# Kernel optimization log

Hardware: AMD Instinct MI355X
Metric: run time of the kernel (lower is better)

## Reference

```python
import jax, jax.numpy as jnp
import numpy as np

B, L, D1, D2 = 4, 2048, 1024, 1024

def setup_inputs() -> dict:
    key = jax.random.key(0)
    k1, k2, k3, k4, k5, k6 = jax.random.split(key, 6)
    s1 = 1.0 / np.sqrt(D1)
    s2 = 1.0 / np.sqrt(D2)
    return {
        "features_1": jax.random.normal(k1, (B, L, D1), dtype=jnp.float32),
        "features_2": jax.random.normal(k2, (B, L, D2), dtype=jnp.float32),
        # nn.Linear(d1, d2): W1 [d2, d1], b1 [d2]
        "W1": jax.random.uniform(k3, (D2, D1), jnp.float32, -s1, s1),
        "b1": jax.random.uniform(k4, (D2,), jnp.float32, -s1, s1),
        # nn.Linear(d2, d1): W2 [d1, d2], b2 [d1]
        "W2": jax.random.uniform(k5, (D1, D2), jnp.float32, -s2, s2),
        "b2": jax.random.uniform(k6, (D1,), jnp.float32, -s2, s2),
    }

def reference(features_1, features_2, W1, b1, W2, b2):
    # transformed_features_1: [B, L, D2]
    t1 = jnp.einsum('bld,ed->ble', features_1, W1) + b1
    # unscaled similarity: [B, L, L]
    sim = jnp.einsum('ble,bme->blm', t1, features_2)
    attn = jax.nn.softmax(sim, axis=-1)  # both softmaxes are identical
    attended_1 = jnp.einsum('blm,bme->ble', attn, features_2)  # [B, L, D2]
    attended_2 = jnp.einsum('blm,bme->ble', attn, t1)          # [B, L, D2]
    attended_2 = jnp.einsum('ble,de->bld', attended_2, W2) + b2  # [B, L, D1]
    return attended_1, attended_2
```

## Files before the change

kernel.cpp:

```cpp
#include <hip/hip_runtime.h>
#include <stdint.h>

#define BB 4
#define LL 2048
#define DD 1024

typedef __attribute__((ext_vector_type(4))) float f32x4;
typedef __attribute__((ext_vector_type(8))) _Float16 f16x8;
typedef __attribute__((ext_vector_type(4))) unsigned short u16x4;
typedef __attribute__((ext_vector_type(8))) unsigned short u16x8;
typedef unsigned short u16;

__device__ __forceinline__ u16 f2h(float x){
  return __builtin_bit_cast(u16, (_Float16)x);
}
__device__ __forceinline__ float h2f(u16 h){
  return (float)__builtin_bit_cast(_Float16, h);
}

__device__ __forceinline__ void gload16(const u16* g, u16* l){
  __builtin_amdgcn_global_load_lds((const __attribute__((address_space(1))) unsigned*)g,
                                   (__attribute__((address_space(3))) unsigned*)l,
                                   16, 0, 0);
}

__device__ __forceinline__ int xcd_swz(int bx, int nwg){
  return (bx & 7) * (nwg >> 3) + (bx >> 3);
}

__device__ __forceinline__ void stage_tile8(u16* lds, const u16* src, int ld, int wave, int lane){
  const int r0 = lane >> 3;
  const int cs = (((lane & 7) ^ r0) << 3);
  #pragma unroll
  for (int j = 0; j < 2; ++j){
    const int rb = wave*16 + j*8;
    gload16(src + (size_t)(rb + r0)*ld + cs, lds + rb*64);
  }
}

__device__ __forceinline__ void stage_fatA(u16* lds, const u16* src, int ld, int wave, int lane){
  const int r0 = lane >> 3;
  const int cs = (((lane & 7) ^ r0) << 3);
  #pragma unroll
  for (int j = 0; j < 8; ++j){
    const int rb = wave*64 + j*8;
    gload16(src + (size_t)(rb + r0)*ld + cs, lds + rb*64);
  }
}
__device__ __forceinline__ void stage_fatB(u16* lds, const u16* src, int ld, int wave, int lane){
  const int r0 = lane >> 3;
  const int cs = (((lane & 7) ^ r0) << 3);
  #pragma unroll
  for (int j = 0; j < 4; ++j){
    const int rb = wave*32 + j*8;
    gload16(src + (size_t)(rb + r0)*ld + cs, lds + rb*64);
  }
}

__device__ __forceinline__ f16x8 frag_ld(const u16* t, int row, int ko){
  return __builtin_bit_cast(f16x8,
    *reinterpret_cast<const f32x4*>(t + row*64 + (ko ^ ((row & 7) << 3))));
}

__global__ void cast_all_k(const float* __restrict__ f2, u16* __restrict__ f2f,
                           u16* __restrict__ f2T,
                           const float* __restrict__ f1, u16* __restrict__ f1f,
                           const float* __restrict__ W1, u16* __restrict__ w1f,
                           const float* __restrict__ W2, u16* __restrict__ w2f){
  __shared__ u16 t[32][33];
  const int z = blockIdx.z;
  if (z < 4){
    const int d0 = blockIdx.x*32, l0 = blockIdx.y*32;
    const float* src = f2 + (size_t)z*LL*DD;
    u16* d1 = f2f + (size_t)z*LL*DD;
    u16* d2 = f2T + (size_t)z*DD*LL;
    const int x = threadIdx.x;
    for (int j = threadIdx.y; j < 32; j += 8){
      u16 h = f2h(src[(size_t)(l0+j)*DD + d0 + x]);
      d1[(size_t)(l0+j)*DD + d0 + x] = h;
      t[j][x] = h;
    }
    __syncthreads();
    for (int j = threadIdx.y; j < 32; j += 8)
      d2[(size_t)(d0+j)*LL + l0 + x] = t[x][j];
  } else {
    const int n1 = (BB*LL*DD)/4, nw = (DD*DD)/4;
    const int ntot = n1 + 2*nw;
    const int base = (blockIdx.y*32 + blockIdx.x)*256 + threadIdx.y*32 + threadIdx.x;
    const int stride = 2048*256;
    for (int i = base; i < ntot; i += stride){
      const float* s; u16* d; int k;
      if (i < n1){ s = f1; d = f1f; k = i; }
      else if (i < n1 + nw){ s = W1; d = w1f; k = i - n1; }
      else { s = W2; d = w2f; k = i - n1 - nw; }
      f32x4 v = reinterpret_cast<const f32x4*>(s)[k];
      u16x4 h;
      #pragma unroll
      for (int j = 0; j < 4; ++j) h[j] = f2h(v[j]);
      reinterpret_cast<u16x4*>(d)[k] = h;
    }
  }
}

__global__ __launch_bounds__(512,4) void gemm_t1_k(
    const u16* __restrict__ A_g, const u16* __restrict__ B_g,
    const float* __restrict__ bias, u16* __restrict__ Oh){
  __shared__ __align__(16) u16 As[128*64];
  __shared__ __align__(16) u16 Bs[128*64];
  const int bx = xcd_swz(blockIdx.x, gridDim.x);
  const int bm = bx >> 3, bn = bx & 7;
  const int tid = threadIdx.x, wave = tid>>6, lane = tid&63;
  const int wr = wave>>2, wc = wave&3;
  const u16* Ab = A_g + (size_t)(bm*128)*DD;
  const u16* Bb = B_g + (size_t)(bn*128)*DD;
  f32x4 acc[4][2];
  #pragma unroll
  for (int i=0;i<4;i++)
    #pragma unroll
    for (int j=0;j<2;j++) acc[i][j] = (f32x4){0.f,0.f,0.f,0.f};

  for (int k0 = 0; k0 < DD; k0 += 64){
    __syncthreads();
    stage_tile8(As, Ab + k0, DD, wave, lane);
    stage_tile8(Bs, Bb + k0, DD, wave, lane);
    __syncthreads();
    #pragma unroll
    for (int kk=0;kk<2;kk++){
      const int ko = kk*32 + ((lane>>4)<<3);
      f16x8 a[4], bb[2];
      #pragma unroll
      for (int mi=0;mi<4;mi++) a[mi]  = frag_ld(As, wr*64 + mi*16 + (lane&15), ko);
      #pragma unroll
      for (int ni=0;ni<2;ni++) bb[ni] = frag_ld(Bs, wc*32 + ni*16 + (lane&15), ko);
      #pragma unroll
      for (int mi=0;mi<4;mi++)
        #pragma unroll
        for (int ni=0;ni<2;ni++)
          acc[mi][ni] = __builtin_amdgcn_mfma_f32_16x16x32_f16(a[mi], bb[ni], acc[mi][ni], 0,0,0);
    }
  }
  #pragma unroll
  for (int mi=0;mi<4;mi++)
    #pragma unroll
    for (int ni=0;ni<2;ni++){
      const int r = bm*128 + wr*64 + mi*16 + ((lane>>4)<<2);
      const int c = bn*128 + wc*32 + ni*16 + (lane&15);
      const float bv = bias[c];
      #pragma unroll
      for (int j=0;j<4;j++)
        Oh[(size_t)(r+j)*DD + c] = f2h(acc[mi][ni][j] + bv);
    }
}

__global__ __launch_bounds__(512,4) void gemm_zt_k(const u16* __restrict__ t1f,
                                                   const u16* __restrict__ w2f,
                                                   u16* __restrict__ ZT){
  __shared__ __align__(16) u16 As[128*64];
  __shared__ __align__(16) u16 Bs[128*64];
  __shared__ u16 T[128*132];
  const int bx = xcd_swz(blockIdx.x, gridDim.x);
  const int bm = bx >> 3, bn = bx & 7;
  const int tid = threadIdx.x, wave = tid>>6, lane = tid&63;
  const int wr = wave>>2, wc = wave&3;
  const u16* Ab = t1f + (size_t)(bm*128)*DD;
  const u16* Bb = w2f + (size_t)(bn*128)*DD;
  f32x4 acc[4][2];
  #pragma unroll
  for (int i=0;i<4;i++)
    #pragma unroll
    for (int j=0;j<2;j++) acc[i][j] = (f32x4){0.f,0.f,0.f,0.f};

  for (int k0 = 0; k0 < DD; k0 += 64){
    __syncthreads();
    stage_tile8(As, Ab + k0, DD, wave, lane);
    stage_tile8(Bs, Bb + k0, DD, wave, lane);
    __syncthreads();
    #pragma unroll
    for (int kk=0;kk<2;kk++){
      const int ko = kk*32 + ((lane>>4)<<3);
      f16x8 a[4], bb[2];
      #pragma unroll
      for (int mi=0;mi<4;mi++) a[mi]  = frag_ld(As, wr*64 + mi*16 + (lane&15), ko);
      #pragma unroll
      for (int ni=0;ni<2;ni++) bb[ni] = frag_ld(Bs, wc*32 + ni*16 + (lane&15), ko);
      #pragma unroll
      for (int mi=0;mi<4;mi++)
        #pragma unroll
        for (int ni=0;ni<2;ni++)
          acc[mi][ni] = __builtin_amdgcn_mfma_f32_16x16x32_f16(a[mi], bb[ni], acc[mi][ni], 0,0,0);
    }
  }
  #pragma unroll
  for (int mi=0;mi<4;mi++)
    #pragma unroll
    for (int ni=0;ni<2;ni++){
      const int r = wr*64 + mi*16 + ((lane>>4)<<2);
      const int c = wc*32 + ni*16 + (lane&15);
      #pragma unroll
      for (int j=0;j<4;j++)
        T[(r+j)*132 + c] = f2h(acc[mi][ni][j]);
    }
  __syncthreads();
  const int b2i = bm >> 4;
  const int mb  = (bm*128) & 2047;
  const int d   = tid >> 2, m0 = (tid & 3) << 5;
  u16* dst = ZT + ((size_t)b2i*DD + bn*128 + d)*LL + mb + m0;
  #pragma unroll
  for (int g = 0; g < 4; ++g){
    u16x8 v;
    #pragma unroll
    for (int e = 0; e < 8; ++e) v[e] = T[(m0 + g*8 + e)*132 + d];
    *reinterpret_cast<u16x8*>(dst + g*8) = v;
  }
}

__global__ __launch_bounds__(256) void softmax_k(u16* __restrict__ sim){
  const int row = blockIdx.x;
  u16* p = sim + (size_t)row * LL;
  const int tid = threadIdx.x, wave = tid>>6, lane = tid&63;
  u16x8 v = reinterpret_cast<const u16x8*>(p)[tid];
  float x[8];
  #pragma unroll
  for (int j=0;j<8;j++) x[j] = h2f(v[j]);
  float mx = fmaxf(fmaxf(fmaxf(x[0],x[1]), fmaxf(x[2],x[3])),
                   fmaxf(fmaxf(x[4],x[5]), fmaxf(x[6],x[7])));
  #pragma unroll
  for (int o = 32; o; o >>= 1) mx = fmaxf(mx, __shfl_xor(mx, o, 64));
  __shared__ float red[8];
  if (lane == 0) red[wave] = mx;
  __syncthreads();
  mx = fmaxf(fmaxf(red[0], red[1]), fmaxf(red[2], red[3]));
  float e[8], s = 0.f;
  #pragma unroll
  for (int j=0;j<8;j++){ e[j] = __expf(x[j]-mx); s += e[j]; }
  #pragma unroll
  for (int o = 32; o; o >>= 1) s += __shfl_xor(s, o, 64);
  if (lane == 0) red[4+wave] = s;
  __syncthreads();
  s = (red[4]+red[5]) + (red[6]+red[7]);
  const float inv = 1.0f / s;
  u16x8 w;
  #pragma unroll
  for (int j=0;j<8;j++) w[j] = f2h(e[j]*inv);
  reinterpret_cast<u16x8*>(p)[tid] = w;
}

template<int EPI>
__global__ __launch_bounds__(256,2) void gemmf_k(
    const u16* __restrict__ A_g, long long sAb, int lda,
    const u16* __restrict__ B0_g, const u16* __restrict__ B1_g, long long sBb, int ldb,
    float* __restrict__ C0, float* __restrict__ C1, long long sCb, int ldc,
    const float* __restrict__ bias, int K, int tn_sh){
  __shared__ __align__(16) u16 As[256*64];
  __shared__ __align__(16) u16 Bs[128*64];
  const int b = blockIdx.y;
  const int bx = xcd_swz(blockIdx.x, gridDim.x);
  const int bm = bx >> tn_sh, bn = bx & ((1 << tn_sh) - 1);
  const int tid = threadIdx.x, wave = tid>>6, lane = tid&63;
  const int wm = wave >> 1, wn = wave & 1;
  const u16* Ab = A_g + (size_t)b*sAb + (size_t)(bm*256)*lda;
  const u16* Bb;
  if (EPI == 1){
    Bb = ((bn < 8) ? B0_g : B1_g) + (size_t)b*sBb + (size_t)((bn&7)*128)*ldb;
  } else {
    Bb = B0_g + (size_t)b*sBb + (size_t)(bn*128)*ldb;
  }
  f32x4 acc[8][4];
  #pragma unroll
  for (int i=0;i<8;i++)
    #pragma unroll
    for (int j=0;j<4;j++) acc[i][j] = (f32x4){0.f,0.f,0.f,0.f};

  for (int k0 = 0; k0 < K; k0 += 64){
    __syncthreads();
    stage_fatA(As, Ab + k0, lda, wave, lane);
    stage_fatB(Bs, Bb + k0, ldb, wave, lane);
    __syncthreads();
    #pragma unroll
    for (int kk=0;kk<2;kk++){
      const int ko = kk*32 + ((lane>>4)<<3);
      f16x8 af[8], bf[4];
      #pragma unroll
      for (int mi=0;mi<8;mi++) af[mi] = frag_ld(As, wm*128 + mi*16 + (lane&15), ko);
      #pragma unroll
      for (int ni=0;ni<4;ni++) bf[ni] = frag_ld(Bs, wn*64 + ni*16 + (lane&15), ko);
      #pragma unroll
      for (int mi=0;mi<8;mi++)
        #pragma unroll
        for (int ni=0;ni<4;ni++)
          acc[mi][ni] = __builtin_amdgcn_mfma_f32_16x16x32_f16(af[mi], bf[ni], acc[mi][ni], 0,0,0);
    }
  }

  if (EPI == 2){
    u16* Oh = reinterpret_cast<u16*>(C0) + (size_t)b*sCb;
    #pragma unroll
    for (int mi=0;mi<8;mi++)
      #pragma unroll
      for (int ni=0;ni<4;ni++){
        const int r = bm*256 + wm*128 + mi*16 + ((lane>>4)<<2);
        const int c = bn*128 + wn*64 + ni*16 + (lane&15);
        #pragma unroll
        for (int j=0;j<4;j++)
          Oh[(size_t)(r+j)*ldc + c] = f2h(acc[mi][ni][j]);
      }
  } else {
    float* O = ((bn < 8) ? C0 : C1) + (size_t)b*sCb;
    const bool has_bias = (bn >= 8);
    #pragma unroll
    for (int mi=0;mi<8;mi++)
      #pragma unroll
      for (int ni=0;ni<4;ni++){
        const int r = bm*256 + wm*128 + mi*16 + ((lane>>4)<<2);
        const int c = (bn&7)*128 + wn*64 + ni*16 + (lane&15);
        const float bv = has_bias ? bias[c] : 0.f;
        #pragma unroll
        for (int j=0;j<4;j++)
          __builtin_nontemporal_store(acc[mi][ni][j] + bv, &O[(size_t)(r+j)*ldc + c]);
      }
  }
}

extern "C" void kernel_launch(void* const* d_in, const int* in_sizes, int n_in,
                              void* d_out, int out_size, void* d_ws, size_t ws_size,
                              hipStream_t stream) {
  const float* f1 = (const float*)d_in[0];
  const float* f2 = (const float*)d_in[1];
  const float* W1 = (const float*)d_in[2];
  const float* b1 = (const float*)d_in[3];
  const float* W2 = (const float*)d_in[4];
  const float* b2 = (const float*)d_in[5];
  float* out1 = (float*)d_out;
  float* out2 = out1 + (size_t)BB*LL*DD;

  char* ws = (char*)d_ws;
  u16* t1f = (u16*)(ws + 0);
  u16* ZT  = (u16*)(ws + 16777216);
  u16* f2f = (u16*)(ws + 33554432);
  u16* f2T = (u16*)(ws + 50331648);
  u16* w1f = (u16*)(ws + 67108864);
  u16* w2f = (u16*)(ws + 69206016);
  u16* sim = (u16*)(ws + 71303168);
  u16* f1f = (u16*)(ws + 71303168);

  cast_all_k<<<dim3(32, 64, 5), dim3(32, 8), 0, stream>>>(f2, f2f, f2T,
                                                          f1, f1f, W1, w1f, W2, w2f);
  gemm_t1_k<<<dim3(512, 1), 512, 0, stream>>>(f1f, w1f, b1, t1f);
  gemmf_k<2><<<dim3(128, BB), 256, 0, stream>>>(t1f, (long long)LL*DD, DD,
                                                f2f, nullptr, (long long)LL*DD, DD,
                                                (float*)sim, nullptr, (long long)LL*LL, LL,
                                                nullptr, DD, 4);
  softmax_k<<<BB*LL, 256, 0, stream>>>(sim);
  gemm_zt_k<<<dim3(512, 1), 512, 0, stream>>>(t1f, w2f, ZT);
  gemmf_k<1><<<dim3(128, BB), 256, 0, stream>>>(sim, (long long)LL*LL, LL,
                                                f2T, ZT, (long long)DD*LL, LL,
                                                out1, out2, (long long)LL*DD, DD,
                                                b2, LL, 4);
}
```

Baseline: 188.5 us.

## Precompute W2·W1 to fuse t1 and Z GEMMs into one pass over f1

Computes W12 = W2·W1 and a folded bias b2 + W2·b1 in small kernels, then a single GEMM kernel reads f1 once and produces both t1 (with W1) and Z^T (with W12). This drops the separate gemm_zt pass that re-read t1 and lets the final attention GEMM use the folded bias. It also adds a transposed cast of W1 and switches the output stores from nontemporal to regular stores. Z is now built from f1 rather than from the fp16-rounded t1, which changes rounding, and the fused kernel uses more LDS and registers per block.

```diff
diff --git a/kernel.cpp b/kernel.cpp
--- a/kernel.cpp
+++ b/kernel.cpp
@@ -64,16 +64,19 @@
 
 __global__ void cast_all_k(const float* __restrict__ f2, u16* __restrict__ f2f,
                            u16* __restrict__ f2T,
+                           const float* __restrict__ W1, u16* __restrict__ w1f,
+                           u16* __restrict__ w1T,
                            const float* __restrict__ f1, u16* __restrict__ f1f,
-                           const float* __restrict__ W1, u16* __restrict__ w1f,
                            const float* __restrict__ W2, u16* __restrict__ w2f){
   __shared__ u16 t[32][33];
   const int z = blockIdx.z;
-  if (z < 4){
+  if (z < 4 || z == 4){
+    const float* src; u16* d1; u16* d2; int nrow, ldT;
+    if (z < 4){ src = f2 + (size_t)z*LL*DD; d1 = f2f + (size_t)z*LL*DD;
+                d2 = f2T + (size_t)z*DD*LL; nrow = LL; ldT = LL; }
+    else      { src = W1; d1 = w1f; d2 = w1T; nrow = DD; ldT = DD; }
     const int d0 = blockIdx.x*32, l0 = blockIdx.y*32;
-    const float* src = f2 + (size_t)z*LL*DD;
-    u16* d1 = f2f + (size_t)z*LL*DD;
-    u16* d2 = f2T + (size_t)z*DD*LL;
+    if (l0 >= nrow) return;
     const int x = threadIdx.x;
     for (int j = threadIdx.y; j < 32; j += 8){
       u16 h = f2h(src[(size_t)(l0+j)*DD + d0 + x]);
@@ -82,17 +85,16 @@
     }
     __syncthreads();
     for (int j = threadIdx.y; j < 32; j += 8)
-      d2[(size_t)(d0+j)*LL + l0 + x] = t[x][j];
+      d2[(size_t)(d0+j)*ldT + l0 + x] = t[x][j];
   } else {
     const int n1 = (BB*LL*DD)/4, nw = (DD*DD)/4;
-    const int ntot = n1 + 2*nw;
+    const int ntot = n1 + nw;
     const int base = (blockIdx.y*32 + blockIdx.x)*256 + threadIdx.y*32 + threadIdx.x;
     const int stride = 2048*256;
     for (int i = base; i < ntot; i += stride){
       const float* s; u16* d; int k;
       if (i < n1){ s = f1; d = f1f; k = i; }
-      else if (i < n1 + nw){ s = W1; d = w1f; k = i - n1; }
-      else { s = W2; d = w2f; k = i - n1 - nw; }
+      else { s = W2; d = w2f; k = i - n1; }
       f32x4 v = reinterpret_cast<const f32x4*>(s)[k];
       u16x4 h;
       #pragma unroll
@@ -102,9 +104,26 @@
   }
 }
 
-__global__ __launch_bounds__(512,4) void gemm_t1_k(
-    const u16* __restrict__ A_g, const u16* __restrict__ B_g,
-    const float* __restrict__ bias, u16* __restrict__ Oh){
+__global__ __launch_bounds__(512) void bz2_k(const float* __restrict__ W2,
+                                             const float* __restrict__ b1,
+                                             const float* __restrict__ b2,
+                                             float* __restrict__ bz2){
+  const int wave = threadIdx.x >> 6, lane = threadIdx.x & 63;
+  const int d = blockIdx.x*8 + wave;
+  float s = 0.f;
+  #pragma unroll
+  for (int k = 0; k < 16; ++k){
+    const int e = lane + (k << 6);
+    s += W2[(size_t)d*DD + e] * b1[e];
+  }
+  #pragma unroll
+  for (int o = 32; o; o >>= 1) s += __shfl_xor(s, o, 64);
+  if (lane == 0) bz2[d] = b2[d] + s;
+}
+
+__global__ __launch_bounds__(512,4) void w12_k(const u16* __restrict__ A_g,
+                                               const u16* __restrict__ B_g,
+                                               u16* __restrict__ Oh){
   __shared__ __align__(16) u16 As[128*64];
   __shared__ __align__(16) u16 Bs[128*64];
   const int bx = xcd_swz(blockIdx.x, gridDim.x);
@@ -118,7 +137,6 @@
   for (int i=0;i<4;i++)
     #pragma unroll
     for (int j=0;j<2;j++) acc[i][j] = (f32x4){0.f,0.f,0.f,0.f};
-
   for (int k0 = 0; k0 < DD; k0 += 64){
     __syncthreads();
     stage_tile8(As, Ab + k0, DD, wave, lane);
@@ -145,51 +163,74 @@
     for (int ni=0;ni<2;ni++){
       const int r = bm*128 + wr*64 + mi*16 + ((lane>>4)<<2);
       const int c = bn*128 + wc*32 + ni*16 + (lane&15);
-      const float bv = bias[c];
       #pragma unroll
       for (int j=0;j<4;j++)
-        Oh[(size_t)(r+j)*DD + c] = f2h(acc[mi][ni][j] + bv);
-    }
-}
-
-__global__ __launch_bounds__(512,4) void gemm_zt_k(const u16* __restrict__ t1f,
-                                                   const u16* __restrict__ w2f,
-                                                   u16* __restrict__ ZT){
-  __shared__ __align__(16) u16 As[128*64];
-  __shared__ __align__(16) u16 Bs[128*64];
-  __shared__ u16 T[128*132];
+        Oh[(size_t)(r+j)*DD + c] = f2h(acc[mi][ni][j]);
+    }
+}
+
+__global__ __launch_bounds__(512,4) void t1z_k(const u16* __restrict__ f1f,
+                                               const u16* __restrict__ w1f,
+                                               const u16* __restrict__ w12f,
+                                               const float* __restrict__ b1,
+                                               u16* __restrict__ t1f,
+                                               u16* __restrict__ ZT){
+  __shared__ __align__(16) u16 SH[3*128*64];
+  u16* As  = SH;
+  u16* B1s = SH + 8192;
+  u16* B2s = SH + 16384;
   const int bx = xcd_swz(blockIdx.x, gridDim.x);
   const int bm = bx >> 3, bn = bx & 7;
   const int tid = threadIdx.x, wave = tid>>6, lane = tid&63;
   const int wr = wave>>2, wc = wave&3;
-  const u16* Ab = t1f + (size_t)(bm*128)*DD;
-  const u16* Bb = w2f + (size_t)(bn*128)*DD;
-  f32x4 acc[4][2];
+  const u16* Ab  = f1f  + (size_t)(bm*128)*DD;
+  const u16* B1b = w1f  + (size_t)(bn*128)*DD;
+  const u16* B2b = w12f + (size_t)(bn*128)*DD;
+  f32x4 acc1[4][2], acc2[4][2];
   #pragma unroll
   for (int i=0;i<4;i++)
     #pragma unroll
-    for (int j=0;j<2;j++) acc[i][j] = (f32x4){0.f,0.f,0.f,0.f};
+    for (int j=0;j<2;j++){ acc1[i][j] = (f32x4){0.f,0.f,0.f,0.f}; acc2[i][j] = acc1[i][j]; }
 
   for (int k0 = 0; k0 < DD; k0 += 64){
     __syncthreads();
-    stage_tile8(As, Ab + k0, DD, wave, lane);
-    stage_tile8(Bs, Bb + k0, DD, wave, lane);
+    stage_tile8(As,  Ab  + k0, DD, wave, lane);
+    stage_tile8(B1s, B1b + k0, DD, wave, lane);
+    stage_tile8(B2s, B2b + k0, DD, wave, lane);
     __syncthreads();
     #pragma unroll
     for (int kk=0;kk<2;kk++){
       const int ko = kk*32 + ((lane>>4)<<3);
-      f16x8 a[4], bb[2];
+      f16x8 a[4], b1v[2], b2v[2];
       #pragma unroll
       for (int mi=0;mi<4;mi++) a[mi]  = frag_ld(As, wr*64 + mi*16 + (lane&15), ko);
       #pragma unroll
-      for (int ni=0;ni<2;ni++) bb[ni] = frag_ld(Bs, wc*32 + ni*16 + (lane&15), ko);
+      for (int ni=0;ni<2;ni++){
+        b1v[ni] = frag_ld(B1s, wc*32 + ni*16 + (lane&15), ko);
+        b2v[ni] = frag_ld(B2s, wc*32 + ni*16 + (lane&15), ko);
+      }
       #pragma unroll
       for (int mi=0;mi<4;mi++)
         #pragma unroll
-        for (int ni=0;ni<2;ni++)
-          acc[mi][ni] = __builtin_amdgcn_mfma_f32_16x16x32_f16(a[mi], bb[ni], acc[mi][ni], 0,0,0);
-    }
-  }
+        for (int ni=0;ni<2;ni++){
+          acc1[mi][ni] = __builtin_amdgcn_mfma_f32_16x16x32_f16(a[mi], b1v[ni], acc1[mi][ni], 0,0,0);
+          acc2[mi][ni] = __builtin_amdgcn_mfma_f32_16x16x32_f16(a[mi], b2v[ni], acc2[mi][ni], 0,0,0);
+        }
+    }
+  }
+  #pragma unroll
+  for (int mi=0;mi<4;mi++)
+    #pragma unroll
+    for (int ni=0;ni<2;ni++){
+      const int r = bm*128 + wr*64 + mi*16 + ((lane>>4)<<2);
+      const int c = bn*128 + wc*32 + ni*16 + (lane&15);
+      const float bv = b1[c];
+      #pragma unroll
+      for (int j=0;j<4;j++)
+        t1f[(size_t)(r+j)*DD + c] = f2h(acc1[mi][ni][j] + bv);
+    }
+  __syncthreads();
+  u16* T = SH;
   #pragma unroll
   for (int mi=0;mi<4;mi++)
     #pragma unroll
@@ -198,7 +239,7 @@
       const int c = wc*32 + ni*16 + (lane&15);
       #pragma unroll
       for (int j=0;j<4;j++)
-        T[(r+j)*132 + c] = f2h(acc[mi][ni][j]);
+        T[(r+j)*132 + c] = f2h(acc2[mi][ni][j]);
     }
   __syncthreads();
   const int b2i = bm >> 4;
@@ -316,7 +357,7 @@
         const float bv = has_bias ? bias[c] : 0.f;
         #pragma unroll
         for (int j=0;j<4;j++)
-          __builtin_nontemporal_store(acc[mi][ni][j] + bv, &O[(size_t)(r+j)*ldc + c]);
+          O[(size_t)(r+j)*ldc + c] = acc[mi][ni][j] + bv;
       }
   }
 }
@@ -341,19 +382,24 @@
   u16* w1f = (u16*)(ws + 67108864);
   u16* w2f = (u16*)(ws + 69206016);
   u16* sim = (u16*)(ws + 71303168);
-  u16* f1f = (u16*)(ws + 71303168);
-
-  cast_all_k<<<dim3(32, 64, 5), dim3(32, 8), 0, stream>>>(f2, f2f, f2T,
-                                                          f1, f1f, W1, w1f, W2, w2f);
-  gemm_t1_k<<<dim3(512, 1), 512, 0, stream>>>(f1f, w1f, b1, t1f);
+  u16* f1f  = (u16*)(ws + 71303168);
+  u16* w1T  = (u16*)(ws + 71303168 + 16777216);
+  u16* w12f = (u16*)(ws + 71303168 + 18874368);
+  float* bz2 = (float*)(ws + 104857600);
+
+  cast_all_k<<<dim3(32, 64, 6), dim3(32, 8), 0, stream>>>(f2, f2f, f2T,
+                                                          W1, w1f, w1T,
+                                                          f1, f1f, W2, w2f);
+  bz2_k<<<128, 512, 0, stream>>>(W2, b1, b2, bz2);
+  w12_k<<<64, 512, 0, stream>>>(w2f, w1T, w12f);
+  t1z_k<<<512, 512, 0, stream>>>(f1f, w1f, w12f, b1, t1f, ZT);
   gemmf_k<2><<<dim3(128, BB), 256, 0, stream>>>(t1f, (long long)LL*DD, DD,
                                                 f2f, nullptr, (long long)LL*DD, DD,
                                                 (float*)sim, nullptr, (long long)LL*LL, LL,
                                                 nullptr, DD, 4);
   softmax_k<<<BB*LL, 256, 0, stream>>>(sim);
-  gemm_zt_k<<<dim3(512, 1), 512, 0, stream>>>(t1f, w2f, ZT);
   gemmf_k<1><<<dim3(128, BB), 256, 0, stream>>>(sim, (long long)LL*LL, LL,
                                                 f2T, ZT, (long long)DD*LL, LL,
                                                 out1, out2, (long long)LL*DD, DD,
-                                                b2, LL, 4);
-}
+                                                bz2, LL, 4);
+}
```

New measurement: 217.7 us. +15.5%, slower.
